# Kernel optimization log

Measured on AMD Instinct MI355X. Metric: run time of the kernel, lower is better.

Reference implementation:

```python
import jax, jax.numpy as jnp
import numpy as np

N, K, E = 50000, 32, 50000 * 32
IN_DIM, FEAT_DIM, HID_DIM, OUT_DIM = 128, 64, 64, 32
EPS = 1e-12  # F.normalize eps


def setup_inputs() -> dict:
    key = jax.random.key(0)
    ks = jax.random.split(key, 16)
    s = 0.1  # small init scale (stand-in for xavier)
    return {
        "feat": jax.random.normal(ks[0], (N, IN_DIM), jnp.float32),
        "dists_max": jax.random.uniform(ks[1], (N, K), jnp.float32),
        "src": jax.random.randint(ks[2], (E,), 0, N, jnp.int32),
        "dst": jax.random.randint(ks[3], (E,), 0, N, jnp.int32),
        "w_pre": jax.random.normal(ks[4], (FEAT_DIM, IN_DIM), jnp.float32) * s,
        "b_pre": jnp.zeros((FEAT_DIM,), jnp.float32),
        "Wu1": jax.random.normal(ks[5], (HID_DIM, FEAT_DIM), jnp.float32) * s,
        "bu1": jnp.zeros((HID_DIM,), jnp.float32),
        "Wv1": jax.random.normal(ks[6], (HID_DIM, FEAT_DIM), jnp.float32) * s,
        "bv1": jnp.zeros((HID_DIM,), jnp.float32),
        "wp1": jax.random.normal(ks[7], (1, HID_DIM), jnp.float32) * s,
        "bp1": jnp.zeros((1,), jnp.float32),
        "Wu2": jax.random.normal(ks[8], (OUT_DIM, HID_DIM), jnp.float32) * s,
        "bu2": jnp.zeros((OUT_DIM,), jnp.float32),
        "Wv2": jax.random.normal(ks[9], (OUT_DIM, HID_DIM), jnp.float32) * s,
        "bv2": jnp.zeros((OUT_DIM,), jnp.float32),
        "wp2": jax.random.normal(ks[10], (1, OUT_DIM), jnp.float32) * s,
        "bp2": jnp.zeros((1,), jnp.float32),
    }


def _pgnn_layer(x, sp_dist, src, dst, Wu, bu, Wv, bv, wp, bp, n, k):
    # x: [N, Din]; sp_dist: [E]; src/dst: [E] (anchor edges, E = N*K)
    u = x @ Wu.T + bu  # [N, D]
    v = x @ Wv.T + bv  # [N, D]
    # u_mul_e then v_add_e: message = v_feat[dst] + u_feat[src] * sp_dist
    msg = v[dst] + u[src] * sp_dist[:, None]          # [E, D]
    msg = jax.nn.relu(msg).reshape(n, k, -1)          # [N, K, D]
    out_position = (msg @ wp.T + bp)[..., 0]          # [N, K]
    out_structure = jnp.mean(msg, axis=1)             # [N, D]
    return out_position, out_structure


def reference(feat, dists_max, src, dst, w_pre, b_pre,
              Wu1, bu1, Wv1, bv1, wp1, bp1,
              Wu2, bu2, Wv2, bv2, wp2, bp2):
    n, k = dists_max.shape
    sp_dist = dists_max.reshape(-1)  # anchor_eid == arange(E): edata sp_dist
    x = feat @ w_pre.T + b_pre  # linear_pre (feature_pre=True)
    _, x = _pgnn_layer(x, sp_dist, src, dst, Wu1, bu1, Wv1, bv1, wp1, bp1, n, k)
    # dropout is identity in eval mode
    x_position, _ = _pgnn_layer(x, sp_dist, src, dst, Wu2, bu2, Wv2, bv2, wp2, bp2, n, k)
    # F.normalize(p=2, dim=-1)
    norm = jnp.maximum(jnp.linalg.norm(x_position, axis=-1, keepdims=True), EPS)
    return x_position / norm
```

## Files before the change

kernel.cpp:

```cpp
#include <hip/hip_runtime.h>

constexpr int NN = 50000;
constexpr int KANCH = 32;

typedef __attribute__((ext_vector_type(8))) short bfrag;
typedef __attribute__((ext_vector_type(4))) float ffrag;

static __device__ __forceinline__ float bf2f(unsigned short u) {
    return __uint_as_float(((unsigned int)u) << 16);
}
static __device__ __forceinline__ unsigned short f2bf(float f) {
    unsigned int x = __float_as_uint(f);
    x += 0x7FFFu + ((x >> 16) & 1u);
    return (unsigned short)(x >> 16);
}

__global__ __launch_bounds__(256) void k_prep(
    const float* __restrict__ w_pre, const float* __restrict__ b_pre,
    const float* __restrict__ Wu1, const float* __restrict__ bu1,
    const float* __restrict__ Wv1, const float* __restrict__ bv1,
    const float* __restrict__ Wu2, const float* __restrict__ bu2,
    const float* __restrict__ Wv2, const float* __restrict__ bv2,
    unsigned short* __restrict__ wcat1, float* __restrict__ bias1,
    unsigned short* __restrict__ wcat2, float* __restrict__ bias2)
{
    int gid = blockIdx.x * 256 + threadIdx.x;
    if (gid < 16384) {
        int j = gid >> 7, i = gid & 127;
        const float* Wr = (j < 64) ? (Wu1 + j * 64) : (Wv1 + (j - 64) * 64);
        float a = 0.f;
        for (int t = 0; t < 64; ++t) a += Wr[t] * w_pre[t * 128 + i];
        wcat1[gid] = f2bf(a);
    } else if (gid < 16384 + 4096) {
        int g = gid - 16384;
        int j = g >> 6, i = g & 63;
        float w = (j < 32) ? Wu2[j * 64 + i] : Wv2[(j - 32) * 64 + i];
        wcat2[g] = f2bf(w);
    } else if (gid < 16384 + 4096 + 128) {
        int j = gid - (16384 + 4096);
        const float* Wr = (j < 64) ? (Wu1 + j * 64) : (Wv1 + (j - 64) * 64);
        float a = (j < 64) ? bu1[j] : bv1[j - 64];
        for (int t = 0; t < 64; ++t) a += Wr[t] * b_pre[t];
        bias1[j] = a;
    } else if (gid < 16384 + 4096 + 128 + 64) {
        int j = gid - (16384 + 4096 + 128);
        bias2[j] = (j < 32) ? bu2[j] : bv2[j - 32];
    }
}

__global__ __launch_bounds__(256) void k_gemm1(
    const float* __restrict__ feat,
    const unsigned short* __restrict__ wcat,
    const float* __restrict__ bias,
    unsigned short* __restrict__ ub,
    unsigned short* __restrict__ vb,
    int nTiles)
{
    __shared__ unsigned short s_w[128 * 136];
    __shared__ float s_b[128];
    int tid = threadIdx.x;
    for (int idx = tid; idx < 128 * 16; idx += 256) {
        int r = idx >> 4, c8 = idx & 15;
        const uint4* g = reinterpret_cast<const uint4*>(wcat + r * 128 + c8 * 8);
        *reinterpret_cast<uint4*>(&s_w[r * 136 + c8 * 8]) = *g;
    }
    if (tid < 128) s_b[tid] = bias[tid];
    __syncthreads();

    int wv = __builtin_amdgcn_readfirstlane(tid >> 6);
    int lane = tid & 63;
    int col = lane & 15;
    int grp = lane >> 4;
    int slot = blockIdx.x * 4 + wv;
    int stride = gridDim.x * 4;
    for (int tile = slot; tile < nTiles; tile += stride) {
        int n0 = tile * 16;
        const float* fp = feat + (size_t)(n0 + col) * 128 + grp * 8;
        bfrag AH[4], AL[4];
#pragma unroll
        for (int s = 0; s < 4; ++s) {
            float4 p0 = *reinterpret_cast<const float4*>(fp + s * 32);
            float4 p1 = *reinterpret_cast<const float4*>(fp + s * 32 + 4);
            float a8[8] = {p0.x, p0.y, p0.z, p0.w, p1.x, p1.y, p1.z, p1.w};
#pragma unroll
            for (int e = 0; e < 8; ++e) {
                unsigned short hb = f2bf(a8[e]);
                AH[s][e] = (short)hb;
                AL[s][e] = (short)f2bf(a8[e] - bf2f(hb));
            }
        }
#pragma unroll
        for (int t = 0; t < 8; ++t) {
            ffrag a = {0.f, 0.f, 0.f, 0.f};
#pragma unroll
            for (int s = 0; s < 4; ++s) {
                const bfrag w = *reinterpret_cast<const bfrag*>(
                    &s_w[(t * 16 + col) * 136 + s * 32 + grp * 8]);
                a = __builtin_amdgcn_mfma_f32_16x16x32_bf16(AH[s], w, a, 0, 0, 0);
                a = __builtin_amdgcn_mfma_f32_16x16x32_bf16(AL[s], w, a, 0, 0, 0);
            }
            float bb = s_b[t * 16 + col];
#pragma unroll
            for (int j = 0; j < 4; ++j) {
                int node = n0 + grp * 4 + j;
                unsigned short o = f2bf(a[j] + bb);
                if (t < 4) ub[(size_t)node * 64 + t * 16 + col] = o;
                else       vb[(size_t)node * 64 + (t - 4) * 16 + col] = o;
            }
        }
    }
}

__global__ __launch_bounds__(256) void k_gather1(
    const ushort4* __restrict__ u1v, const ushort4* __restrict__ v1v,
    const int* __restrict__ src, const int* __restrict__ dst,
    const float* __restrict__ dists, ushort4* __restrict__ x2v)
{
    int tid = threadIdx.x;
    int wv = __builtin_amdgcn_readfirstlane(tid >> 6);
    int lane = tid & 63;
    int c = lane & 15;
    int es = lane >> 4;
    int slot = blockIdx.x * 4 + wv;
    int stride = gridDim.x * 4;
    for (int n = slot; n < NN; n += stride) {
        int base = n * KANCH;
        float a0 = 0.f, a1 = 0.f, a2 = 0.f, a3 = 0.f;
#pragma unroll
        for (int kk = 0; kk < 8; ++kk) {
            int k = kk * 4 + es;
            int sk = src[base + k];
            int dk = dst[base + k];
            float sp = dists[base + k];
            ushort4 uu = u1v[(size_t)sk * 16 + c];
            ushort4 vv = v1v[(size_t)dk * 16 + c];
            a0 += fmaxf(fmaf(bf2f(uu.x), sp, bf2f(vv.x)), 0.f);
            a1 += fmaxf(fmaf(bf2f(uu.y), sp, bf2f(vv.y)), 0.f);
            a2 += fmaxf(fmaf(bf2f(uu.z), sp, bf2f(vv.z)), 0.f);
            a3 += fmaxf(fmaf(bf2f(uu.w), sp, bf2f(vv.w)), 0.f);
        }
        a0 += __shfl_xor(a0, 16); a0 += __shfl_xor(a0, 32);
        a1 += __shfl_xor(a1, 16); a1 += __shfl_xor(a1, 32);
        a2 += __shfl_xor(a2, 16); a2 += __shfl_xor(a2, 32);
        a3 += __shfl_xor(a3, 16); a3 += __shfl_xor(a3, 32);
        if (lane < 16) {
            ushort4 r;
            r.x = f2bf(a0 * 0.03125f); r.y = f2bf(a1 * 0.03125f);
            r.z = f2bf(a2 * 0.03125f); r.w = f2bf(a3 * 0.03125f);
            x2v[(size_t)n * 16 + c] = r;
        }
    }
}

__global__ __launch_bounds__(256) void k_gemm2(
    const unsigned short* __restrict__ x2b,
    const unsigned short* __restrict__ wcat,
    const float* __restrict__ bias,
    unsigned short* __restrict__ ub,
    unsigned short* __restrict__ vb,
    int nTiles)
{
    __shared__ unsigned short s_w[64 * 72];
    __shared__ float s_b[64];
    int tid = threadIdx.x;
    for (int idx = tid; idx < 64 * 8; idx += 256) {
        int r = idx >> 3, c8 = idx & 7;
        const uint4* g = reinterpret_cast<const uint4*>(wcat + r * 64 + c8 * 8);
        *reinterpret_cast<uint4*>(&s_w[r * 72 + c8 * 8]) = *g;
    }
    if (tid < 64) s_b[tid] = bias[tid];
    __syncthreads();

    int wv = __builtin_amdgcn_readfirstlane(tid >> 6);
    int lane = tid & 63;
    int col = lane & 15;
    int grp = lane >> 4;
    int slot = blockIdx.x * 4 + wv;
    int stride = gridDim.x * 4;
    for (int tile = slot; tile < nTiles; tile += stride) {
        int n0 = tile * 16;
        bfrag A[2];
#pragma unroll
        for (int s = 0; s < 2; ++s) {
            uint4 raw = *reinterpret_cast<const uint4*>(
                x2b + (size_t)(n0 + col) * 64 + s * 32 + grp * 8);
            A[s] = *reinterpret_cast<const bfrag*>(&raw);
        }
#pragma unroll
        for (int t = 0; t < 4; ++t) {
            ffrag a = {0.f, 0.f, 0.f, 0.f};
#pragma unroll
            for (int s = 0; s < 2; ++s) {
                const bfrag w = *reinterpret_cast<const bfrag*>(
                    &s_w[(t * 16 + col) * 72 + s * 32 + grp * 8]);
                a = __builtin_amdgcn_mfma_f32_16x16x32_bf16(A[s], w, a, 0, 0, 0);
            }
            float bb = s_b[t * 16 + col];
#pragma unroll
            for (int j = 0; j < 4; ++j) {
                int node = n0 + grp * 4 + j;
                unsigned short o = f2bf(a[j] + bb);
                if (t < 2) ub[(size_t)node * 32 + t * 16 + col] = o;
                else       vb[(size_t)node * 32 + (t - 2) * 16 + col] = o;
            }
        }
    }
}

__global__ __launch_bounds__(256) void k_out(
    const ushort4* __restrict__ u2v, const ushort4* __restrict__ v2v,
    const int* __restrict__ src, const int* __restrict__ dst,
    const float* __restrict__ dists, const float* __restrict__ wp2,
    const float* __restrict__ bp2, float* __restrict__ out)
{
    int tid = threadIdx.x;
    int wv = __builtin_amdgcn_readfirstlane(tid >> 6);
    int lane = tid & 63;
    int c = lane & 7;
    int es = lane >> 3;
    int slot = blockIdx.x * 4 + wv;
    int stride = gridDim.x * 4;
    float4 w4 = reinterpret_cast<const float4*>(wp2)[c];
    float bp = bp2[0];
    for (int n = slot; n < NN; n += stride) {
        int base = n * KANCH;
        float q0, q1, q2, q3;
#pragma unroll
        for (int kk = 0; kk < 4; ++kk) {
            int k = kk * 8 + es;
            int sk = src[base + k];
            int dk = dst[base + k];
            float sp = dists[base + k];
            ushort4 uu = u2v[(size_t)sk * 8 + c];
            ushort4 vv = v2v[(size_t)dk * 8 + c];
            float p;
            p  = fmaxf(fmaf(bf2f(uu.x), sp, bf2f(vv.x)), 0.f) * w4.x;
            p += fmaxf(fmaf(bf2f(uu.y), sp, bf2f(vv.y)), 0.f) * w4.y;
            p += fmaxf(fmaf(bf2f(uu.z), sp, bf2f(vv.z)), 0.f) * w4.z;
            p += fmaxf(fmaf(bf2f(uu.w), sp, bf2f(vv.w)), 0.f) * w4.w;
            p += __shfl_xor(p, 1);
            p += __shfl_xor(p, 2);
            p += __shfl_xor(p, 4);
            if (kk == 0) q0 = p; else if (kk == 1) q1 = p;
            else if (kk == 2) q2 = p; else q3 = p;
        }
        int srcl = (lane & 7) * 8;
        float s0 = __shfl(q0, srcl);
        float s1 = __shfl(q1, srcl);
        float s2_ = __shfl(q2, srcl);
        float s3 = __shfl(q3, srcl);
        int it = (lane >> 3) & 3;
        float q = (it == 0) ? s0 : (it == 1) ? s1 : (it == 2) ? s2_ : s3;
        q += bp;
        float ss = q * q;
#pragma unroll
        for (int off = 16; off >= 1; off >>= 1)
            ss += __shfl_xor(ss, off);
        float den = fmaxf(sqrtf(ss), 1e-12f);
        if (lane < 32) out[(size_t)n * KANCH + lane] = q / den;
    }
}

extern "C" void kernel_launch(void* const* d_in, const int* in_sizes, int n_in,
                              void* d_out, int out_size, void* d_ws, size_t ws_size,
                              hipStream_t stream)
{
    const float* feat  = (const float*)d_in[0];
    const float* dists = (const float*)d_in[1];
    const int*   src   = (const int*)d_in[2];
    const int*   dst   = (const int*)d_in[3];
    const float* w_pre = (const float*)d_in[4];
    const float* b_pre = (const float*)d_in[5];
    const float* Wu1   = (const float*)d_in[6];
    const float* bu1   = (const float*)d_in[7];
    const float* Wv1   = (const float*)d_in[8];
    const float* bv1   = (const float*)d_in[9];
    const float* Wu2   = (const float*)d_in[12];
    const float* bu2   = (const float*)d_in[13];
    const float* Wv2   = (const float*)d_in[14];
    const float* bv2   = (const float*)d_in[15];
    const float* wp2   = (const float*)d_in[16];
    const float* bp2   = (const float*)d_in[17];
    float* out = (float*)d_out;

    unsigned short* wcat1 = (unsigned short*)d_ws;
    float* bias1 = (float*)(wcat1 + 16384);
    unsigned short* wcat2 = (unsigned short*)(bias1 + 128);
    float* bias2 = (float*)(wcat2 + 4096);
    unsigned short* u1b = (unsigned short*)(bias2 + 64);
    unsigned short* v1b = u1b + (size_t)NN * 64;
    unsigned short* x2b = v1b + (size_t)NN * 64;
    unsigned short* u2b = u1b;
    unsigned short* v2b = v1b;

    k_prep<<<81, 256, 0, stream>>>(w_pre, b_pre, Wu1, bu1, Wv1, bv1,
                                   Wu2, bu2, Wv2, bv2,
                                   wcat1, bias1, wcat2, bias2);
    k_gemm1<<<782, 256, 0, stream>>>(feat, wcat1, bias1, u1b, v1b, NN / 16);
    k_gather1<<<2048, 256, 0, stream>>>((const ushort4*)u1b, (const ushort4*)v1b,
                                        src, dst, dists, (ushort4*)x2b);
    k_gemm2<<<782, 256, 0, stream>>>(x2b, wcat2, bias2, u2b, v2b, NN / 16);
    k_out<<<2048, 256, 0, stream>>>((const ushort4*)u2b, (const ushort4*)v2b,
                                    src, dst, dists, wp2, bp2, out);
}
```

Before: 108.8 us.

## Slice layer-1 u/v by column into four planes and gather per slice

GEMM1 now writes u1/v1 as four column-sliced planes of 16 features each, and the layer-1 gather runs as four launches, one per slice. The aim is to keep each slice's random-gather working set (about 1.6 MB per tensor) resident in L2, instead of gathering full 128-byte rows from the whole table. Index and distance loads are made nontemporal in both gather kernels. In exchange, src, dst and dists are re-read four times, there are three extra kernel launches, and each gathered access is only 8 bytes.

Result: slower. 181.3 us (+66.7%).

```diff
diff --git a/kernel.cpp b/kernel.cpp
--- a/kernel.cpp
+++ b/kernel.cpp
@@ -52,8 +52,8 @@
     const float* __restrict__ feat,
     const unsigned short* __restrict__ wcat,
     const float* __restrict__ bias,
-    unsigned short* __restrict__ ub,
-    unsigned short* __restrict__ vb,
+    unsigned short* __restrict__ u1s,
+    unsigned short* __restrict__ v1s,
     int nTiles)
 {
     __shared__ unsigned short s_w[128 * 136];
@@ -104,50 +104,56 @@
             for (int j = 0; j < 4; ++j) {
                 int node = n0 + grp * 4 + j;
                 unsigned short o = f2bf(a[j] + bb);
-                if (t < 4) ub[(size_t)node * 64 + t * 16 + col] = o;
-                else       vb[(size_t)node * 64 + (t - 4) * 16 + col] = o;
-            }
-        }
-    }
-}
-
-__global__ __launch_bounds__(256) void k_gather1(
-    const ushort4* __restrict__ u1v, const ushort4* __restrict__ v1v,
+                if (t < 4) u1s[((size_t)t * NN + node) * 16 + col] = o;
+                else       v1s[((size_t)(t - 4) * NN + node) * 16 + col] = o;
+            }
+        }
+    }
+}
+
+__global__ __launch_bounds__(256) void k_gather1s(
+    const ushort4* __restrict__ u1s, const ushort4* __restrict__ v1s,
     const int* __restrict__ src, const int* __restrict__ dst,
-    const float* __restrict__ dists, ushort4* __restrict__ x2v)
+    const float* __restrict__ dists, ushort4* __restrict__ x2v,
+    int slice)
 {
     int tid = threadIdx.x;
     int wv = __builtin_amdgcn_readfirstlane(tid >> 6);
     int lane = tid & 63;
-    int c = lane & 15;
-    int es = lane >> 4;
+    int c = lane & 3;
+    int es = lane >> 2;
     int slot = blockIdx.x * 4 + wv;
     int stride = gridDim.x * 4;
+    size_t tbase = (size_t)slice * NN * 4;
     for (int n = slot; n < NN; n += stride) {
         int base = n * KANCH;
         float a0 = 0.f, a1 = 0.f, a2 = 0.f, a3 = 0.f;
 #pragma unroll
-        for (int kk = 0; kk < 8; ++kk) {
-            int k = kk * 4 + es;
-            int sk = src[base + k];
-            int dk = dst[base + k];
-            float sp = dists[base + k];
-            ushort4 uu = u1v[(size_t)sk * 16 + c];
-            ushort4 vv = v1v[(size_t)dk * 16 + c];
+        for (int kk = 0; kk < 2; ++kk) {
+            int k = kk * 16 + es;
+            int sk = __builtin_nontemporal_load(src + base + k);
+            int dk = __builtin_nontemporal_load(dst + base + k);
+            float sp = __builtin_nontemporal_load(dists + base + k);
+            ushort4 uu = u1s[tbase + (size_t)sk * 4 + c];
+            ushort4 vv = v1s[tbase + (size_t)dk * 4 + c];
             a0 += fmaxf(fmaf(bf2f(uu.x), sp, bf2f(vv.x)), 0.f);
             a1 += fmaxf(fmaf(bf2f(uu.y), sp, bf2f(vv.y)), 0.f);
             a2 += fmaxf(fmaf(bf2f(uu.z), sp, bf2f(vv.z)), 0.f);
             a3 += fmaxf(fmaf(bf2f(uu.w), sp, bf2f(vv.w)), 0.f);
         }
+        a0 += __shfl_xor(a0, 4); a0 += __shfl_xor(a0, 8);
         a0 += __shfl_xor(a0, 16); a0 += __shfl_xor(a0, 32);
+        a1 += __shfl_xor(a1, 4); a1 += __shfl_xor(a1, 8);
         a1 += __shfl_xor(a1, 16); a1 += __shfl_xor(a1, 32);
+        a2 += __shfl_xor(a2, 4); a2 += __shfl_xor(a2, 8);
         a2 += __shfl_xor(a2, 16); a2 += __shfl_xor(a2, 32);
+        a3 += __shfl_xor(a3, 4); a3 += __shfl_xor(a3, 8);
         a3 += __shfl_xor(a3, 16); a3 += __shfl_xor(a3, 32);
-        if (lane < 16) {
+        if (lane < 4) {
             ushort4 r;
             r.x = f2bf(a0 * 0.03125f); r.y = f2bf(a1 * 0.03125f);
             r.z = f2bf(a2 * 0.03125f); r.w = f2bf(a3 * 0.03125f);
-            x2v[(size_t)n * 16 + c] = r;
+            x2v[(size_t)n * 16 + slice * 4 + lane] = r;
         }
     }
 }
@@ -228,9 +234,9 @@
 #pragma unroll
         for (int kk = 0; kk < 4; ++kk) {
             int k = kk * 8 + es;
-            int sk = src[base + k];
-            int dk = dst[base + k];
-            float sp = dists[base + k];
+            int sk = __builtin_nontemporal_load(src + base + k);
+            int dk = __builtin_nontemporal_load(dst + base + k);
+            float sp = __builtin_nontemporal_load(dists + base + k);
             ushort4 uu = u2v[(size_t)sk * 8 + c];
             ushort4 vv = v2v[(size_t)dk * 8 + c];
             float p;
@@ -287,18 +293,19 @@
     float* bias1 = (float*)(wcat1 + 16384);
     unsigned short* wcat2 = (unsigned short*)(bias1 + 128);
     float* bias2 = (float*)(wcat2 + 4096);
-    unsigned short* u1b = (unsigned short*)(bias2 + 64);
-    unsigned short* v1b = u1b + (size_t)NN * 64;
-    unsigned short* x2b = v1b + (size_t)NN * 64;
-    unsigned short* u2b = u1b;
-    unsigned short* v2b = v1b;
+    unsigned short* u1s = (unsigned short*)(bias2 + 64);
+    unsigned short* v1s = u1s + (size_t)NN * 64;
+    unsigned short* x2b = v1s + (size_t)NN * 64;
+    unsigned short* u2b = u1s;
+    unsigned short* v2b = v1s;
 
     k_prep<<<81, 256, 0, stream>>>(w_pre, b_pre, Wu1, bu1, Wv1, bv1,
                                    Wu2, bu2, Wv2, bv2,
                                    wcat1, bias1, wcat2, bias2);
-    k_gemm1<<<782, 256, 0, stream>>>(feat, wcat1, bias1, u1b, v1b, NN / 16);
-    k_gather1<<<2048, 256, 0, stream>>>((const ushort4*)u1b, (const ushort4*)v1b,
-                                        src, dst, dists, (ushort4*)x2b);
+    k_gemm1<<<782, 256, 0, stream>>>(feat, wcat1, bias1, u1s, v1s, NN / 16);
+    for (int s = 0; s < 4; ++s)
+        k_gather1s<<<2048, 256, 0, stream>>>((const ushort4*)u1s, (const ushort4*)v1s,
+                                             src, dst, dists, (ushort4*)x2b, s);
     k_gemm2<<<782, 256, 0, stream>>>(x2b, wcat2, bias2, u2b, v2b, NN / 16);
     k_out<<<2048, 256, 0, stream>>>((const ushort4*)u2b, (const ushort4*)v2b,
                                     src, dst, dists, wp2, bp2, out);
```
